# Optimization experiments

Measured on AMD Instinct MI355X. Metric: run time of the kernel, lower is better.

The kernel has to match this reference:

```python
import jax, jax.numpy as jnp
import numpy as np

N = 100000      # nodes
E = 1600000     # edges
C_IN = 128
H = 64          # hidden_channels
FC = [128, 64, 32, 16]
G = 64          # graphs in batch
EPS = 1e-5


def _glorot(key, fan_in, fan_out):
    s = 1.0 / np.sqrt(fan_in)
    return jax.random.uniform(key, (fan_in, fan_out), jnp.float32, -s, s)


def setup_inputs() -> dict:
    key = jax.random.key(0)
    ks = jax.random.split(key, 24)
    inp = {
        "x": jax.random.normal(ks[0], (N, C_IN), jnp.float32),
        "edge_index": jax.random.randint(ks[1], (2, E), 0, N, jnp.int32),
        "batch": jnp.sort(jax.random.randint(ks[2], (N,), 0, G, jnp.int32)),
        # GCN layers
        "W1": _glorot(ks[3], C_IN, H), "b1": jnp.zeros((H,), jnp.float32),
        "W2": _glorot(ks[4], H, H),    "b2": jnp.zeros((H,), jnp.float32),
        # BatchNorm affine params
        "gamma1": jnp.ones((H,), jnp.float32), "beta1": jnp.zeros((H,), jnp.float32),
        "gamma2": jnp.ones((H,), jnp.float32), "beta2": jnp.zeros((H,), jnp.float32),
        # MLP stack 64->128->64->32->16->1
        "fW1": _glorot(ks[5], H, FC[0]),     "fb1": jnp.zeros((FC[0],), jnp.float32),
        "fW2": _glorot(ks[6], FC[0], FC[1]), "fb2": jnp.zeros((FC[1],), jnp.float32),
        "fW3": _glorot(ks[7], FC[1], FC[2]), "fb3": jnp.zeros((FC[2],), jnp.float32),
        "fW4": _glorot(ks[8], FC[2], FC[3]), "fb4": jnp.zeros((FC[3],), jnp.float32),
        "oW": _glorot(ks[9], FC[3], 1),      "ob": jnp.zeros((1,), jnp.float32),
    }
    return inp


def gcn_conv(x, W, b, src, dst):
    # x' = D^{-1/2} (A + I) D^{-1/2} X W + b   (PyG GCNConv, add_self_loops=True)
    h = x @ W                                             # [N, H]
    loops = jnp.arange(N, dtype=src.dtype)
    s = jnp.concatenate([src, loops])
    d = jnp.concatenate([dst, loops])
    deg = jax.ops.segment_sum(jnp.ones_like(d, jnp.float32), d, num_segments=N)
    dinv = jax.lax.rsqrt(deg)                             # deg >= 1 (self-loops)
    norm = dinv[s] * dinv[d]                              # [E+N]
    msg = h[s] * norm[:, None]                            # gather + scale
    return jax.ops.segment_sum(msg, d, num_segments=N) + b


def batch_norm(x, gamma, beta):
    mu = jnp.mean(x, axis=0)
    var = jnp.mean((x - mu) ** 2, axis=0)                 # biased, as torch BN
    return (x - mu) * jax.lax.rsqrt(var + EPS) * gamma + beta


def reference(x, edge_index, batch, W1, b1, W2, b2, gamma1, beta1, gamma2, beta2,
              fW1, fb1, fW2, fb2, fW3, fb3, fW4, fb4, oW, ob):
    src, dst = edge_index[0], edge_index[1]
    h = jax.nn.relu(gcn_conv(x, W1, b1, src, dst))
    h = batch_norm(h, gamma1, beta1)                      # dropout = identity (eval)
    h = jax.nn.relu(gcn_conv(h, W2, b2, src, dst))
    h = batch_norm(h, gamma2, beta2)
    # global mean pool over graphs
    sums = jax.ops.segment_sum(h, batch, num_segments=G)
    cnts = jax.ops.segment_sum(jnp.ones((N,), jnp.float32), batch, num_segments=G)
    g = sums / jnp.maximum(cnts, 1.0)[:, None]            # [G, H]
    g = jax.nn.relu(g @ fW1 + fb1)
    g = jax.nn.relu(g @ fW2 + fb2)
    g = jax.nn.relu(g @ fW3 + fb3)
    g = jax.nn.relu(g @ fW4 + fb4)
    return g @ oW + ob                                    # [G, 1]
```

## Files before the change

### kernel.cpp

```cpp
#include <hip/hip_runtime.h>
#include <hip/hip_bf16.h>
#include <hip/hip_fp16.h>

#define NNODES 100000
#define NEDGES 1600000
#define NGRAPH 64
#define NCOPY  32
#define NSLOT  8

#define CAP     48
#define NGEMM1  1563

#define PSH     9
#define PSZ2    512
#define NP2     196
#define PCAP    9216

__global__ __launch_bounds__(256) void k_bucket_gemm1(const float* __restrict__ A,
                                                      const float* __restrict__ W,
                                                      const int* __restrict__ ei,
                                                      unsigned* __restrict__ pstage,
                                                      unsigned* __restrict__ pcur,
                                                      __half* __restrict__ hd) {
    __shared__ __align__(16) float smem[64 * 64 + 64 * 68];
    const int b   = blockIdx.x;
    const int tid = threadIdx.x;

    if (b & 1) {
        unsigned* lcnt  = reinterpret_cast<unsigned*>(smem);
        unsigned* lbase = lcnt + 256;
        if (tid < NP2) lcnt[tid] = 0u;
        __syncthreads();

        int e = (b >> 1) * 1024 + tid * 4;
        bool valid = (e < NEDGES);
        unsigned v0=0,v1=0,v2=0,v3=0, p0=0,p1=0,p2=0,p3=0, o0=0,o1=0,o2=0,o3=0;
        if (valid) {
            int4 sv = *reinterpret_cast<const int4*>(&ei[e]);
            int4 dv = *reinterpret_cast<const int4*>(&ei[NEDGES + e]);
            unsigned d;
            d = (unsigned)dv.x; p0 = d >> PSH; v0 = ((d & (PSZ2-1u)) << 17) | (unsigned)sv.x; o0 = atomicAdd(&lcnt[p0], 1u);
            d = (unsigned)dv.y; p1 = d >> PSH; v1 = ((d & (PSZ2-1u)) << 17) | (unsigned)sv.y; o1 = atomicAdd(&lcnt[p1], 1u);
            d = (unsigned)dv.z; p2 = d >> PSH; v2 = ((d & (PSZ2-1u)) << 17) | (unsigned)sv.z; o2 = atomicAdd(&lcnt[p2], 1u);
            d = (unsigned)dv.w; p3 = d >> PSH; v3 = ((d & (PSZ2-1u)) << 17) | (unsigned)sv.w; o3 = atomicAdd(&lcnt[p3], 1u);
        }
        __syncthreads();
        if (tid < NP2) {
            unsigned c = lcnt[tid];
            lbase[tid] = c ? atomicAdd(&pcur[tid], c) : 0u;
        }
        __syncthreads();
        if (valid) {
            unsigned i0 = lbase[p0] + o0; if (i0 < PCAP) pstage[(size_t)p0 * PCAP + i0] = v0;
            unsigned i1 = lbase[p1] + o1; if (i1 < PCAP) pstage[(size_t)p1 * PCAP + i1] = v1;
            unsigned i2 = lbase[p2] + o2; if (i2 < PCAP) pstage[(size_t)p2 * PCAP + i2] = v2;
            unsigned i3 = lbase[p3] + o3; if (i3 < PCAP) pstage[(size_t)p3 * PCAP + i3] = v3;
        }
        return;
    }

    float* wlds = smem;
    float* alds = smem + 64 * 64;
    const int tc = (tid & 15) * 4;
    const int tr = (tid >> 4) * 4;
    const int row0 = (b >> 1) * 64;
    float acc[4][4];
    #pragma unroll
    for (int i = 0; i < 4; ++i)
        #pragma unroll
        for (int j = 0; j < 4; ++j) acc[i][j] = 0.f;

    for (int kc = 0; kc < 2; ++kc) {
        for (int idx2 = tid; idx2 < 64 * 16; idx2 += 256) {
            int r = idx2 >> 4, kk = (idx2 & 15) * 4;
            *reinterpret_cast<float4*>(&wlds[r * 64 + kk]) =
                *reinterpret_cast<const float4*>(&W[(kc * 64 + r) * 64 + kk]);
        }
        for (int idx2 = tid; idx2 < 64 * 16; idx2 += 256) {
            int r = idx2 >> 4, kk = (idx2 & 15) * 4;
            int row = row0 + r;
            float4 v = make_float4(0.f, 0.f, 0.f, 0.f);
            if (row < NNODES) v = *reinterpret_cast<const float4*>(&A[(size_t)row * 128 + kc * 64 + kk]);
            *reinterpret_cast<float4*>(&alds[r * 68 + kk]) = v;
        }
        __syncthreads();
        #pragma unroll 8
        for (int k = 0; k < 64; ++k) {
            float4 wv = *reinterpret_cast<const float4*>(&wlds[k * 64 + tc]);
            float av[4];
            #pragma unroll
            for (int i = 0; i < 4; ++i) av[i] = alds[(tr + i) * 68 + k];
            #pragma unroll
            for (int i = 0; i < 4; ++i) {
                acc[i][0] = fmaf(av[i], wv.x, acc[i][0]);
                acc[i][1] = fmaf(av[i], wv.y, acc[i][1]);
                acc[i][2] = fmaf(av[i], wv.z, acc[i][2]);
                acc[i][3] = fmaf(av[i], wv.w, acc[i][3]);
            }
        }
        __syncthreads();
    }
    #pragma unroll
    for (int i = 0; i < 4; ++i) {
        int row = row0 + tr + i;
        if (row < NNODES) {
            __half2* p = reinterpret_cast<__half2*>(&hd[(size_t)row * 64 + tc]);
            p[0] = __floats2half2_rn(acc[i][0], acc[i][1]);
            p[1] = __floats2half2_rn(acc[i][2], acc[i][3]);
        }
    }
}

__global__ __launch_bounds__(1024) void k_build(const unsigned* __restrict__ pstage,
                                                const unsigned* __restrict__ pcur,
                                                unsigned* __restrict__ cnt,
                                                float* __restrict__ dinv,
                                                unsigned* __restrict__ colidx) {
    const int p   = blockIdx.x;
    const int tid = threadIdx.x;
    __shared__ unsigned cl[PSZ2];
    if (tid < PSZ2) cl[tid] = 0u;
    __syncthreads();
    unsigned nedge = min(pcur[p], (unsigned)PCAP);
    const unsigned* q = &pstage[(size_t)p * PCAP];
    for (unsigned i = tid; i < nedge; i += 1024) {
        unsigned v    = q[i];
        unsigned r    = v >> 17;
        unsigned src  = v & 0x1FFFFu;
        unsigned slot = atomicAdd(&cl[r], 1u);
        unsigned node = ((unsigned)p << PSH) + r;
        if (slot < CAP) colidx[node * CAP + slot] = src;
    }
    __syncthreads();
    if (tid < PSZ2) {
        unsigned node = ((unsigned)p << PSH) + (unsigned)tid;
        if (node < NNODES) {
            unsigned c = cl[tid];
            cnt[node]  = c;
            dinv[node] = rsqrtf((float)(c + 1u));
        }
    }
}

__device__ __forceinline__ void acc_row(const __half* __restrict__ hd, unsigned s, int c0, float4& acc) {
    uint2 u = *reinterpret_cast<const uint2*>(&hd[(size_t)s * 64 + c0]);
    __half2 x01 = *reinterpret_cast<__half2*>(&u.x);
    __half2 x23 = *reinterpret_cast<__half2*>(&u.y);
    float2 f01 = __half22float2(x01);
    float2 f23 = __half22float2(x23);
    acc.x += f01.x; acc.y += f01.y; acc.z += f23.x; acc.w += f23.y;
}
__device__ __forceinline__ void acc_row_s(const __half* __restrict__ hd, const float* __restrict__ dinv,
                                          unsigned s, int c0, float4& acc) {
    float ds = dinv[s];
    uint2 u = *reinterpret_cast<const uint2*>(&hd[(size_t)s * 64 + c0]);
    __half2 x01 = *reinterpret_cast<__half2*>(&u.x);
    __half2 x23 = *reinterpret_cast<__half2*>(&u.y);
    float2 f01 = __half22float2(x01);
    float2 f23 = __half22float2(x23);
    acc.x = fmaf(f01.x, ds, acc.x); acc.y = fmaf(f01.y, ds, acc.y);
    acc.z = fmaf(f23.x, ds, acc.z); acc.w = fmaf(f23.y, ds, acc.w);
}

#define WAVE_REDUCE_8(s0,s1,s2,s3,q0,q1,q2,q3)                      \
    {                                                                \
        _Pragma("unroll")                                            \
        for (int m = 16; m < 64; m <<= 1) {                          \
            s0 += __shfl_xor(s0, m); s1 += __shfl_xor(s1, m);        \
            s2 += __shfl_xor(s2, m); s3 += __shfl_xor(s3, m);        \
            q0 += __shfl_xor(q0, m); q1 += __shfl_xor(q1, m);        \
            q2 += __shfl_xor(q2, m); q3 += __shfl_xor(q3, m);        \
        }                                                            \
    }

__global__ __launch_bounds__(256) void k_gather_fused(const unsigned* __restrict__ cnt,
                                                      const unsigned* __restrict__ colidx,
                                                      const __half* __restrict__ hd,
                                                      const float* __restrict__ dinv,
                                                      const float* __restrict__ bias,
                                                      __half* __restrict__ acth,
                                                      float* bn_sum, float* bn_sq, int n) {
    const int tid = threadIdx.x;
    const int grp = tid >> 4;
    const int c0  = (tid & 15) * 4;
    float4 bv = *reinterpret_cast<const float4*>(&bias[c0]);
    float s0=0.f,s1=0.f,s2=0.f,s3=0.f, q0=0.f,q1=0.f,q2=0.f,q3=0.f;

    #pragma unroll
    for (int it = 0; it < 2; ++it) {
        int node = blockIdx.x * 32 + grp * 2 + it;
        if (node < n) {
            unsigned deg = cnt[node];
            unsigned lo = (unsigned)node * CAP;
            unsigned hi = lo + deg;
            float4 acc = make_float4(0.f, 0.f, 0.f, 0.f);
            acc_row_s(hd, dinv, (unsigned)node, c0, acc);
            unsigned j = lo;
            for (; j + 4 <= hi; j += 4) {
                uint4 a = *reinterpret_cast<const uint4*>(&colidx[j]);
                acc_row_s(hd, dinv, a.x, c0, acc);
                acc_row_s(hd, dinv, a.y, c0, acc);
                acc_row_s(hd, dinv, a.z, c0, acc);
                acc_row_s(hd, dinv, a.w, c0, acc);
            }
            for (; j < hi; ++j) acc_row_s(hd, dinv, colidx[j], c0, acc);
            float w = dinv[node];
            float4 r;
            r.x = fmaxf(fmaf(acc.x, w, bv.x), 0.f);
            r.y = fmaxf(fmaf(acc.y, w, bv.y), 0.f);
            r.z = fmaxf(fmaf(acc.z, w, bv.z), 0.f);
            r.w = fmaxf(fmaf(acc.w, w, bv.w), 0.f);
            __half2* pa = reinterpret_cast<__half2*>(&acth[(size_t)node * 64 + c0]);
            pa[0] = __floats2half2_rn(r.x, r.y);
            pa[1] = __floats2half2_rn(r.z, r.w);
            s0 += r.x; s1 += r.y; s2 += r.z; s3 += r.w;
            q0 = fmaf(r.x, r.x, q0); q1 = fmaf(r.y, r.y, q1);
            q2 = fmaf(r.z, r.z, q2); q3 = fmaf(r.w, r.w, q3);
        }
    }

    WAVE_REDUCE_8(s0,s1,s2,s3,q0,q1,q2,q3);
    __shared__ float ls[4 * 64];
    __shared__ float lq[4 * 64];
    int lane = tid & 63, wid = tid >> 6;
    if (lane < 16) {
        *reinterpret_cast<float4*>(&ls[wid * 64 + lane * 4]) = make_float4(s0, s1, s2, s3);
        *reinterpret_cast<float4*>(&lq[wid * 64 + lane * 4]) = make_float4(q0, q1, q2, q3);
    }
    __syncthreads();
    if (tid < 64) {
        int cpy = (blockIdx.x & (NCOPY - 1)) * 64;
        float S = ls[tid] + ls[64 + tid] + ls[128 + tid] + ls[192 + tid];
        float Q = lq[tid] + lq[64 + tid] + lq[128 + tid] + lq[192 + tid];
        atomicAdd(&bn_sum[cpy + tid], S);
        atomicAdd(&bn_sq[cpy + tid],  Q);
    }
}

__global__ __launch_bounds__(256) void k_gemm2_fold(const __half* __restrict__ A,
                                                    const float* __restrict__ W2,
                                                    const float* __restrict__ bn_sum,
                                                    const float* __restrict__ bn_sq,
                                                    const float* __restrict__ gamma,
                                                    const float* __restrict__ beta,
                                                    const float* __restrict__ rowscale,
                                                    __half* __restrict__ hd, int n) {
    __shared__ float wlds[64 * 64];
    __shared__ float alds[64 * 68];
    __shared__ float scs[64], shs[64], c2s[64];
    const int tid = threadIdx.x;
    const int tc  = (tid & 15) * 4;
    const int tr  = (tid >> 4) * 4;
    const int row0 = blockIdx.x * 64;

    if (tid < 64) {
        float S = 0.f, Q = 0.f;
        #pragma unroll
        for (int cpy = 0; cpy < NCOPY; ++cpy) { S += bn_sum[cpy * 64 + tid]; Q += bn_sq[cpy * 64 + tid]; }
        float inv_n = 1.0f / (float)n;
        float mu  = S * inv_n;
        float var = Q * inv_n - mu * mu;
        float s = gamma[tid] * rsqrtf(var + 1e-5f);
        scs[tid] = s; shs[tid] = beta[tid] - mu * s;
    }
    __syncthreads();
    for (int idx = tid; idx < 4096; idx += 256) {
        int k = idx >> 6;
        wlds[idx] = scs[k] * W2[idx];
    }
    if (tid < 64) {
        float acc = 0.f;
        for (int k = 0; k < 64; ++k) acc = fmaf(shs[k], W2[k * 64 + tid], acc);
        c2s[tid] = acc;
    }
    for (int idx = tid; idx < 64 * 16; idx += 256) {
        int r = idx >> 4, kk = (idx & 15) * 4;
        int row = row0 + r;
        float4 v = make_float4(0.f, 0.f, 0.f, 0.f);
        if (row < n) {
            uint2 u = *reinterpret_cast<const uint2*>(&A[(size_t)row * 64 + kk]);
            __half2 h01 = *reinterpret_cast<__half2*>(&u.x);
            __half2 h23 = *reinterpret_cast<__half2*>(&u.y);
            float2 f01 = __half22float2(h01);
            float2 f23 = __half22float2(h23);
            v = make_float4(f01.x, f01.y, f23.x, f23.y);
        }
        *reinterpret_cast<float4*>(&alds[r * 68 + kk]) = v;
    }
    __syncthreads();

    float acc[4][4];
    float4 cv = make_float4(c2s[tc], c2s[tc + 1], c2s[tc + 2], c2s[tc + 3]);
    #pragma unroll
    for (int i = 0; i < 4; ++i) { acc[i][0]=cv.x; acc[i][1]=cv.y; acc[i][2]=cv.z; acc[i][3]=cv.w; }

    #pragma unroll 8
    for (int k = 0; k < 64; ++k) {
        float4 wv = *reinterpret_cast<const float4*>(&wlds[k * 64 + tc]);
        float av[4];
        #pragma unroll
        for (int i = 0; i < 4; ++i) av[i] = alds[(tr + i) * 68 + k];
        #pragma unroll
        for (int i = 0; i < 4; ++i) {
            acc[i][0] = fmaf(av[i], wv.x, acc[i][0]);
            acc[i][1] = fmaf(av[i], wv.y, acc[i][1]);
            acc[i][2] = fmaf(av[i], wv.z, acc[i][2]);
            acc[i][3] = fmaf(av[i], wv.w, acc[i][3]);
        }
    }
    #pragma unroll
    for (int i = 0; i < 4; ++i) {
        int row = row0 + tr + i;
        if (row < n) {
            float f = rowscale[row];
            __half2* p = reinterpret_cast<__half2*>(&hd[(size_t)row * 64 + tc]);
            p[0] = __floats2half2_rn(acc[i][0] * f, acc[i][1] * f);
            p[1] = __floats2half2_rn(acc[i][2] * f, acc[i][3] * f);
        }
    }
}

__global__ __launch_bounds__(256) void k_gather_pool(const unsigned* __restrict__ cnt,
                                                     const unsigned* __restrict__ colidx,
                                                     const __half* __restrict__ hd,
                                                     const float* __restrict__ dinv,
                                                     const float* __restrict__ bias,
                                                     const int* __restrict__ batch,
                                                     float* __restrict__ gsum,
                                                     float* bn_sum, float* bn_sq, int n) {
    const int tid = threadIdx.x;
    const int grp = tid >> 4;
    const int c0  = (tid & 15) * 4;
    float4 bv = *reinterpret_cast<const float4*>(&bias[c0]);
    float s0=0.f,s1=0.f,s2=0.f,s3=0.f, q0=0.f,q1=0.f,q2=0.f,q3=0.f;

    __shared__ float lds_pool[NSLOT * 64];
    for (int i = tid; i < NSLOT * 64; i += 256) lds_pool[i] = 0.f;
    int node0 = blockIdx.x * 32;
    int g0 = batch[node0 < n ? node0 : (n - 1)];
    __syncthreads();

    #pragma unroll
    for (int it = 0; it < 2; ++it) {
        int node = node0 + grp * 2 + it;
        if (node < n) {
            unsigned deg = cnt[node];
            unsigned lo = (unsigned)node * CAP;
            unsigned hi = lo + deg;
            float4 acc = make_float4(0.f, 0.f, 0.f, 0.f);
            acc_row(hd, (unsigned)node, c0, acc);
            unsigned j = lo;
            for (; j + 4 <= hi; j += 4) {
                uint4 a = *reinterpret_cast<const uint4*>(&colidx[j]);
                acc_row(hd, a.x, c0, acc);
                acc_row(hd, a.y, c0, acc);
                acc_row(hd, a.z, c0, acc);
                acc_row(hd, a.w, c0, acc);
            }
            for (; j < hi; ++j) acc_row(hd, colidx[j], c0, acc);
            float w = dinv[node];
            float4 r;
            r.x = fmaxf(fmaf(acc.x, w, bv.x), 0.f);
            r.y = fmaxf(fmaf(acc.y, w, bv.y), 0.f);
            r.z = fmaxf(fmaf(acc.z, w, bv.z), 0.f);
            r.w = fmaxf(fmaf(acc.w, w, bv.w), 0.f);
            s0 += r.x; s1 += r.y; s2 += r.z; s3 += r.w;
            q0 = fmaf(r.x, r.x, q0); q1 = fmaf(r.y, r.y, q1);
            q2 = fmaf(r.z, r.z, q2); q3 = fmaf(r.w, r.w, q3);
            int slot = batch[node] - g0;
            if (slot < NSLOT) {
                atomicAdd(&lds_pool[slot * 64 + c0 + 0], r.x);
                atomicAdd(&lds_pool[slot * 64 + c0 + 1], r.y);
                atomicAdd(&lds_pool[slot * 64 + c0 + 2], r.z);
                atomicAdd(&lds_pool[slot * 64 + c0 + 3], r.w);
            } else {
                int g = g0 + slot;
                atomicAdd(&gsum[g * 64 + c0 + 0], r.x);
                atomicAdd(&gsum[g * 64 + c0 + 1], r.y);
                atomicAdd(&gsum[g * 64 + c0 + 2], r.z);
                atomicAdd(&gsum[g * 64 + c0 + 3], r.w);
            }
        }
    }

    WAVE_REDUCE_8(s0,s1,s2,s3,q0,q1,q2,q3);
    __shared__ float ls[4 * 64];
    __shared__ float lq[4 * 64];
    int lane = tid & 63, wid = tid >> 6;
    if (lane < 16) {
        *reinterpret_cast<float4*>(&ls[wid * 64 + lane * 4]) = make_float4(s0, s1, s2, s3);
        *reinterpret_cast<float4*>(&lq[wid * 64 + lane * 4]) = make_float4(q0, q1, q2, q3);
    }
    __syncthreads();
    if (tid < 64) {
        int cpy = (blockIdx.x & (NCOPY - 1)) * 64;
        float S = ls[tid] + ls[64 + tid] + ls[128 + tid] + ls[192 + tid];
        float Q = lq[tid] + lq[64 + tid] + lq[128 + tid] + lq[192 + tid];
        atomicAdd(&bn_sum[cpy + tid], S);
        atomicAdd(&bn_sq[cpy + tid],  Q);
        #pragma unroll
        for (int sl = 0; sl < NSLOT; ++sl) {
            int g = g0 + sl;
            if (g < NGRAPH) {
                float v = lds_pool[sl * 64 + tid];
                if (v != 0.f) atomicAdd(&gsum[g * 64 + tid], v);
            }
        }
    }
}

__device__ __forceinline__ int lower_bound_i(const int* a, int n, int v) {
    int lo = 0, hi = n;
    while (lo < hi) { int m = (lo + hi) >> 1; if (a[m] < v) lo = m + 1; else hi = m; }
    return lo;
}
__global__ __launch_bounds__(128) void k_mlp(const float* __restrict__ gsum,
                                             const int* __restrict__ batch, int n,
                                             const float* __restrict__ bn_sum, const float* __restrict__ bn_sq,
                                             const float* __restrict__ gamma, const float* __restrict__ beta,
                                             const float* __restrict__ fW1, const float* __restrict__ fb1,
                                             const float* __restrict__ fW2, const float* __restrict__ fb2,
                                             const float* __restrict__ fW3, const float* __restrict__ fb3,
                                             const float* __restrict__ fW4, const float* __restrict__ fb4,
                                             const float* __restrict__ oW,  const float* __restrict__ ob,
                                             float* __restrict__ out) {
    int g = blockIdx.x;
    int t = threadIdx.x;
    __shared__ float a[128], bbuf[128];
    if (t < 64) {
        float S = 0.f, Q = 0.f;
        #pragma unroll
        for (int cpy = 0; cpy < NCOPY; ++cpy) { S += bn_sum[cpy * 64 + t]; Q += bn_sq[cpy * 64 + t]; }
        float inv_n = 1.0f / (float)n;
        float mu  = S * inv_n;
        float var = Q * inv_n - mu * mu;
        float s   = gamma[t] * rsqrtf(var + 1e-5f);
        float sh  = beta[t] - mu * s;
        int lo = lower_bound_i(batch, n, g);
        int hi = lower_bound_i(batch, n, g + 1);
        int cnt = hi - lo;
        a[t] = (cnt > 0) ? (gsum[g * 64 + t] / (float)cnt) * s + sh : 0.f;
    }
    __syncthreads();
    {
        float acc = fb1[t];
        for (int k = 0; k < 64; ++k) acc = fmaf(a[k], fW1[k * 128 + t], acc);
        bbuf[t] = fmaxf(acc, 0.f);
    }
    __syncthreads();
    if (t < 64) {
        float acc = fb2[t];
        for (int k = 0; k < 128; ++k) acc = fmaf(bbuf[k], fW2[k * 64 + t], acc);
        a[t] = fmaxf(acc, 0.f);
    }
    __syncthreads();
    if (t < 32) {
        float acc = fb3[t];
        for (int k = 0; k < 64; ++k) acc = fmaf(a[k], fW3[k * 32 + t], acc);
        bbuf[t] = fmaxf(acc, 0.f);
    }
    __syncthreads();
    if (t < 16) {
        float acc = fb4[t];
        for (int k = 0; k < 32; ++k) acc = fmaf(bbuf[k], fW4[k * 16 + t], acc);
        a[t] = fmaxf(acc, 0.f);
    }
    __syncthreads();
    if (t == 0) {
        float acc = ob[0];
        for (int k = 0; k < 16; ++k) acc = fmaf(a[k], oW[k], acc);
        out[g] = acc;
    }
}

extern "C" void kernel_launch(void* const* d_in, const int* in_sizes, int n_in,
                              void* d_out, int out_size, void* d_ws, size_t ws_size,
                              hipStream_t stream) {
    const float* x      = (const float*)d_in[0];
    const int*   ei     = (const int*)  d_in[1];
    const int*   batch  = (const int*)  d_in[2];
    const float* W1     = (const float*)d_in[3];
    const float* b1     = (const float*)d_in[4];
    const float* W2     = (const float*)d_in[5];
    const float* b2     = (const float*)d_in[6];
    const float* gamma1 = (const float*)d_in[7];
    const float* beta1  = (const float*)d_in[8];
    const float* gamma2 = (const float*)d_in[9];
    const float* beta2  = (const float*)d_in[10];
    const float* fW1    = (const float*)d_in[11];
    const float* fb1    = (const float*)d_in[12];
    const float* fW2    = (const float*)d_in[13];
    const float* fb2    = (const float*)d_in[14];
    const float* fW3    = (const float*)d_in[15];
    const float* fb3    = (const float*)d_in[16];
    const float* fW4    = (const float*)d_in[17];
    const float* fb4    = (const float*)d_in[18];
    const float* oW     = (const float*)d_in[19];
    const float* ob     = (const float*)d_in[20];
    float* out = (float*)d_out;

    const int N = NNODES, G = NGRAPH;

    char* base = (char*)d_ws;
    __half*   hd     = (__half*)base;
    __half*   acth   = (__half*)(base + (size_t)N * 64 * 2);
    unsigned* cnt    = (unsigned*)(base + (size_t)N * 64 * 4);
    float*    dinv   = (float*)(cnt + N);
    unsigned* colidx = (unsigned*)(dinv + N);
    float*    bn1s   = (float*)(colidx + (size_t)N * CAP);
    float*    bn1q   = bn1s + NCOPY * 64;
    float*    bn2s   = bn1q + NCOPY * 64;
    float*    bn2q   = bn2s + NCOPY * 64;
    float*    gsum   = bn2q + NCOPY * 64;
    unsigned* pcur   = (unsigned*)(gsum + (size_t)G * 64);
    const size_t ZBYTES = (size_t)(4 * NCOPY * 64 + G * 64) * 4 + (size_t)NP2 * 4;
    unsigned* pstage = (unsigned*)acth;

    hipMemsetAsync(bn1s, 0, ZBYTES, stream);

    k_bucket_gemm1<<<2 * NGEMM1, 256, 0, stream>>>(x, W1, ei, pstage, pcur, hd);

    k_build<<<NP2, 1024, 0, stream>>>(pstage, pcur, cnt, dinv, colidx);

    k_gather_fused<<<(N + 31) / 32, 256, 0, stream>>>(cnt, colidx, hd, dinv, b1, acth, bn1s, bn1q, N);

    k_gemm2_fold<<<NGEMM1, 256, 0, stream>>>(acth, W2, bn1s, bn1q, gamma1, beta1, dinv, hd, N);

    k_gather_pool<<<(N + 31) / 32, 256, 0, stream>>>(cnt, colidx, hd, dinv, b2, batch, gsum, bn2s, bn2q, N);

    k_mlp<<<G, 128, 0, stream>>>(gsum, batch, N, bn2s, bn2q, gamma2, beta2,
                                 fW1, fb1, fW2, fb2, fW3, fb3, fW4, fb4, oW, ob, out);
}
```

Before: 306.1 us.

## Split bucketing from GEMM1 and fold source dinv scaling into GEMM1 output

Edge bucketing now runs as its own kernel with 1024-thread blocks covering 4096 edges each, and the first-layer GEMM moves after the CSR build. Because dinv is then known, the GEMM scales each output row by its dinv before storing fp16. The first gather therefore drops its per-neighbour dinv load and FMA and does plain adds. The cost is that GEMM1 no longer overlaps with bucketing inside one launch, and there is one extra kernel launch.

```diff
diff --git a/kernel.cpp b/kernel.cpp
--- a/kernel.cpp
+++ b/kernel.cpp
@@ -15,55 +15,85 @@
 #define PSZ2    512
 #define NP2     196
 #define PCAP    9216
-
-__global__ __launch_bounds__(256) void k_bucket_gemm1(const float* __restrict__ A,
-                                                      const float* __restrict__ W,
-                                                      const int* __restrict__ ei,
-                                                      unsigned* __restrict__ pstage,
-                                                      unsigned* __restrict__ pcur,
-                                                      __half* __restrict__ hd) {
-    __shared__ __align__(16) float smem[64 * 64 + 64 * 68];
-    const int b   = blockIdx.x;
+#define EPB     4096
+#define NBP1    391
+
+__global__ __launch_bounds__(1024) void k_bucket(const int* __restrict__ ei,
+                                                 unsigned* __restrict__ pstage,
+                                                 unsigned* __restrict__ pcur) {
     const int tid = threadIdx.x;
-
-    if (b & 1) {
-        unsigned* lcnt  = reinterpret_cast<unsigned*>(smem);
-        unsigned* lbase = lcnt + 256;
-        if (tid < NP2) lcnt[tid] = 0u;
-        __syncthreads();
-
-        int e = (b >> 1) * 1024 + tid * 4;
-        bool valid = (e < NEDGES);
-        unsigned v0=0,v1=0,v2=0,v3=0, p0=0,p1=0,p2=0,p3=0, o0=0,o1=0,o2=0,o3=0;
-        if (valid) {
-            int4 sv = *reinterpret_cast<const int4*>(&ei[e]);
-            int4 dv = *reinterpret_cast<const int4*>(&ei[NEDGES + e]);
-            unsigned d;
-            d = (unsigned)dv.x; p0 = d >> PSH; v0 = ((d & (PSZ2-1u)) << 17) | (unsigned)sv.x; o0 = atomicAdd(&lcnt[p0], 1u);
-            d = (unsigned)dv.y; p1 = d >> PSH; v1 = ((d & (PSZ2-1u)) << 17) | (unsigned)sv.y; o1 = atomicAdd(&lcnt[p1], 1u);
-            d = (unsigned)dv.z; p2 = d >> PSH; v2 = ((d & (PSZ2-1u)) << 17) | (unsigned)sv.z; o2 = atomicAdd(&lcnt[p2], 1u);
-            d = (unsigned)dv.w; p3 = d >> PSH; v3 = ((d & (PSZ2-1u)) << 17) | (unsigned)sv.w; o3 = atomicAdd(&lcnt[p3], 1u);
-        }
-        __syncthreads();
-        if (tid < NP2) {
-            unsigned c = lcnt[tid];
-            lbase[tid] = c ? atomicAdd(&pcur[tid], c) : 0u;
-        }
-        __syncthreads();
-        if (valid) {
-            unsigned i0 = lbase[p0] + o0; if (i0 < PCAP) pstage[(size_t)p0 * PCAP + i0] = v0;
-            unsigned i1 = lbase[p1] + o1; if (i1 < PCAP) pstage[(size_t)p1 * PCAP + i1] = v1;
-            unsigned i2 = lbase[p2] + o2; if (i2 < PCAP) pstage[(size_t)p2 * PCAP + i2] = v2;
-            unsigned i3 = lbase[p3] + o3; if (i3 < PCAP) pstage[(size_t)p3 * PCAP + i3] = v3;
-        }
-        return;
-    }
-
-    float* wlds = smem;
-    float* alds = smem + 64 * 64;
+    __shared__ unsigned lcnt[NP2];
+    __shared__ unsigned lbase[NP2];
+    if (tid < NP2) lcnt[tid] = 0u;
+    __syncthreads();
+
+    int e = blockIdx.x * EPB + tid * 4;
+    bool valid = (e < NEDGES);
+    unsigned v0=0,v1=0,v2=0,v3=0, p0=0,p1=0,p2=0,p3=0, o0=0,o1=0,o2=0,o3=0;
+    if (valid) {
+        int4 sv = *reinterpret_cast<const int4*>(&ei[e]);
+        int4 dv = *reinterpret_cast<const int4*>(&ei[NEDGES + e]);
+        unsigned d;
+        d = (unsigned)dv.x; p0 = d >> PSH; v0 = ((d & (PSZ2-1u)) << 17) | (unsigned)sv.x; o0 = atomicAdd(&lcnt[p0], 1u);
+        d = (unsigned)dv.y; p1 = d >> PSH; v1 = ((d & (PSZ2-1u)) << 17) | (unsigned)sv.y; o1 = atomicAdd(&lcnt[p1], 1u);
+        d = (unsigned)dv.z; p2 = d >> PSH; v2 = ((d & (PSZ2-1u)) << 17) | (unsigned)sv.z; o2 = atomicAdd(&lcnt[p2], 1u);
+        d = (unsigned)dv.w; p3 = d >> PSH; v3 = ((d & (PSZ2-1u)) << 17) | (unsigned)sv.w; o3 = atomicAdd(&lcnt[p3], 1u);
+    }
+    __syncthreads();
+    if (tid < NP2) {
+        unsigned c = lcnt[tid];
+        lbase[tid] = c ? atomicAdd(&pcur[tid], c) : 0u;
+    }
+    __syncthreads();
+    if (valid) {
+        unsigned i0 = lbase[p0] + o0; if (i0 < PCAP) pstage[(size_t)p0 * PCAP + i0] = v0;
+        unsigned i1 = lbase[p1] + o1; if (i1 < PCAP) pstage[(size_t)p1 * PCAP + i1] = v1;
+        unsigned i2 = lbase[p2] + o2; if (i2 < PCAP) pstage[(size_t)p2 * PCAP + i2] = v2;
+        unsigned i3 = lbase[p3] + o3; if (i3 < PCAP) pstage[(size_t)p3 * PCAP + i3] = v3;
+    }
+}
+
+__global__ __launch_bounds__(1024) void k_build(const unsigned* __restrict__ pstage,
+                                                const unsigned* __restrict__ pcur,
+                                                unsigned* __restrict__ cnt,
+                                                float* __restrict__ dinv,
+                                                unsigned* __restrict__ colidx) {
+    const int p   = blockIdx.x;
+    const int tid = threadIdx.x;
+    __shared__ unsigned cl[PSZ2];
+    if (tid < PSZ2) cl[tid] = 0u;
+    __syncthreads();
+    unsigned nedge = min(pcur[p], (unsigned)PCAP);
+    const unsigned* q = &pstage[(size_t)p * PCAP];
+    for (unsigned i = tid; i < nedge; i += 1024) {
+        unsigned v    = q[i];
+        unsigned r    = v >> 17;
+        unsigned src  = v & 0x1FFFFu;
+        unsigned slot = atomicAdd(&cl[r], 1u);
+        unsigned node = ((unsigned)p << PSH) + r;
+        if (slot < CAP) colidx[node * CAP + slot] = src;
+    }
+    __syncthreads();
+    if (tid < PSZ2) {
+        unsigned node = ((unsigned)p << PSH) + (unsigned)tid;
+        if (node < NNODES) {
+            unsigned c = cl[tid];
+            cnt[node]  = c;
+            dinv[node] = rsqrtf((float)(c + 1u));
+        }
+    }
+}
+
+__global__ __launch_bounds__(256) void k_gemm1(const float* __restrict__ A,
+                                               const float* __restrict__ W,
+                                               const float* __restrict__ rowscale,
+                                               __half* __restrict__ hd) {
+    __shared__ float wlds[64 * 64];
+    __shared__ float alds[64 * 68];
+    const int tid = threadIdx.x;
     const int tc = (tid & 15) * 4;
     const int tr = (tid >> 4) * 4;
-    const int row0 = (b >> 1) * 64;
+    const int row0 = blockIdx.x * 64;
     float acc[4][4];
     #pragma unroll
     for (int i = 0; i < 4; ++i)
@@ -104,40 +134,10 @@
     for (int i = 0; i < 4; ++i) {
         int row = row0 + tr + i;
         if (row < NNODES) {
+            float f = rowscale[row];
             __half2* p = reinterpret_cast<__half2*>(&hd[(size_t)row * 64 + tc]);
-            p[0] = __floats2half2_rn(acc[i][0], acc[i][1]);
-            p[1] = __floats2half2_rn(acc[i][2], acc[i][3]);
-        }
-    }
-}
-
-__global__ __launch_bounds__(1024) void k_build(const unsigned* __restrict__ pstage,
-                                                const unsigned* __restrict__ pcur,
-                                                unsigned* __restrict__ cnt,
-                                                float* __restrict__ dinv,
-                                                unsigned* __restrict__ colidx) {
-    const int p   = blockIdx.x;
-    const int tid = threadIdx.x;
-    __shared__ unsigned cl[PSZ2];
-    if (tid < PSZ2) cl[tid] = 0u;
-    __syncthreads();
-    unsigned nedge = min(pcur[p], (unsigned)PCAP);
-    const unsigned* q = &pstage[(size_t)p * PCAP];
-    for (unsigned i = tid; i < nedge; i += 1024) {
-        unsigned v    = q[i];
-        unsigned r    = v >> 17;
-        unsigned src  = v & 0x1FFFFu;
-        unsigned slot = atomicAdd(&cl[r], 1u);
-        unsigned node = ((unsigned)p << PSH) + r;
-        if (slot < CAP) colidx[node * CAP + slot] = src;
-    }
-    __syncthreads();
-    if (tid < PSZ2) {
-        unsigned node = ((unsigned)p << PSH) + (unsigned)tid;
-        if (node < NNODES) {
-            unsigned c = cl[tid];
-            cnt[node]  = c;
-            dinv[node] = rsqrtf((float)(c + 1u));
+            p[0] = __floats2half2_rn(acc[i][0] * f, acc[i][1] * f);
+            p[1] = __floats2half2_rn(acc[i][2] * f, acc[i][3] * f);
         }
     }
 }
@@ -149,17 +149,6 @@
     float2 f01 = __half22float2(x01);
     float2 f23 = __half22float2(x23);
     acc.x += f01.x; acc.y += f01.y; acc.z += f23.x; acc.w += f23.y;
-}
-__device__ __forceinline__ void acc_row_s(const __half* __restrict__ hd, const float* __restrict__ dinv,
-                                          unsigned s, int c0, float4& acc) {
-    float ds = dinv[s];
-    uint2 u = *reinterpret_cast<const uint2*>(&hd[(size_t)s * 64 + c0]);
-    __half2 x01 = *reinterpret_cast<__half2*>(&u.x);
-    __half2 x23 = *reinterpret_cast<__half2*>(&u.y);
-    float2 f01 = __half22float2(x01);
-    float2 f23 = __half22float2(x23);
-    acc.x = fmaf(f01.x, ds, acc.x); acc.y = fmaf(f01.y, ds, acc.y);
-    acc.z = fmaf(f23.x, ds, acc.z); acc.w = fmaf(f23.y, ds, acc.w);
 }
 
 #define WAVE_REDUCE_8(s0,s1,s2,s3,q0,q1,q2,q3)                      \
@@ -194,16 +183,16 @@
             unsigned lo = (unsigned)node * CAP;
             unsigned hi = lo + deg;
             float4 acc = make_float4(0.f, 0.f, 0.f, 0.f);
-            acc_row_s(hd, dinv, (unsigned)node, c0, acc);
+            acc_row(hd, (unsigned)node, c0, acc);
             unsigned j = lo;
             for (; j + 4 <= hi; j += 4) {
                 uint4 a = *reinterpret_cast<const uint4*>(&colidx[j]);
-                acc_row_s(hd, dinv, a.x, c0, acc);
-                acc_row_s(hd, dinv, a.y, c0, acc);
-                acc_row_s(hd, dinv, a.z, c0, acc);
-                acc_row_s(hd, dinv, a.w, c0, acc);
+                acc_row(hd, a.x, c0, acc);
+                acc_row(hd, a.y, c0, acc);
+                acc_row(hd, a.z, c0, acc);
+                acc_row(hd, a.w, c0, acc);
             }
-            for (; j < hi; ++j) acc_row_s(hd, dinv, colidx[j], c0, acc);
+            for (; j < hi; ++j) acc_row(hd, colidx[j], c0, acc);
             float w = dinv[node];
             float4 r;
             r.x = fmaxf(fmaf(acc.x, w, bv.x), 0.f);
@@ -518,9 +507,11 @@
 
     hipMemsetAsync(bn1s, 0, ZBYTES, stream);
 
-    k_bucket_gemm1<<<2 * NGEMM1, 256, 0, stream>>>(x, W1, ei, pstage, pcur, hd);
+    k_bucket<<<NBP1, 1024, 0, stream>>>(ei, pstage, pcur);
 
     k_build<<<NP2, 1024, 0, stream>>>(pstage, pcur, cnt, dinv, colidx);
+
+    k_gemm1<<<NGEMM1, 256, 0, stream>>>(x, W1, dinv, hd);
 
     k_gather_fused<<<(N + 31) / 32, 256, 0, stream>>>(cnt, colidx, hd, dinv, b1, acth, bn1s, bn1q, N);
 
```

Result: no change. 305.9 us, median of 2 (-0.1%).
